# Kernel tuning notes

Measured on AMD Instinct MI355X. Metric: run time of the kernel, lower is better.

## Reference

```python
import jax, jax.numpy as jnp
import numpy as np

DIM = 48
HEADS = 8
DIM1 = DIM * HEADS  # 384
RED = 16


def setup_inputs() -> dict:
    key = jax.random.key(0)
    ks = jax.random.split(key, 10)
    s = 0.02
    return {
        "x": jax.random.normal(ks[0], (4, DIM, 128, 128), dtype=jnp.float32),
        "qkv_w": jax.random.normal(ks[1], (DIM1 * 4, DIM), dtype=jnp.float32) * s,
        "dw_w": jax.random.normal(ks[2], (DIM1 * 4, HEADS, 3, 3), dtype=jnp.float32) * s,  # groups=DIM*4 -> 8 in-ch per group
        "po1_w": jax.random.normal(ks[3], (DIM, DIM1), dtype=jnp.float32) * s,
        "fc1_w": jax.random.normal(ks[4], (DIM1 // RED, DIM1), dtype=jnp.float32) * s,
        "fc1_b": jnp.zeros((DIM1 // RED,), dtype=jnp.float32),
        "fc2_w": jax.random.normal(ks[5], (DIM1, DIM1 // RED), dtype=jnp.float32) * s,
        "fc2_b": jnp.zeros((DIM1,), dtype=jnp.float32),
        "temperature": jnp.ones((HEADS, 1, 1), dtype=jnp.float32),
    }


def reference(x, qkv_w, dw_w, po1_w, fc1_w, fc1_b, fc2_w, fc2_b, temperature):
    b, c, h, w = x.shape  # c == dim
    heads = temperature.shape[0]
    # 1x1 pointwise conv: dim -> dim1*4
    qkv = jnp.einsum('bchw,oc->bohw', x, qkv_w)
    # grouped 3x3 conv, groups = dim*4 (8 channels per group)
    qkv = jax.lax.conv_general_dilated(
        qkv, dw_w, window_strides=(1, 1), padding='SAME',
        feature_group_count=c * 4,
        dimension_numbers=('NCHW', 'OIHW', 'NCHW'))
    q, k, v, l = jnp.split(qkv, 4, axis=1)  # each (b, dim1, h, w)
    hw = h * w
    q = q.reshape(b, heads, c, hw)
    k = k.reshape(b, heads, c, hw)
    v = v.reshape(b, heads, c, hw)
    # ChannelAttention on l: note it returns fc2_out * sigmoid(fc2_out)
    avg = jnp.mean(l, axis=(2, 3))  # (b, dim1)
    y = jax.nn.relu(avg @ fc1_w.T + fc1_b)
    y = y @ fc2_w.T + fc2_b  # (b, dim1)
    L = (y * jax.nn.sigmoid(y))[:, :, None, None]  # (b, dim1, 1, 1)
    # L2-normalize over spatial (last) axis, torch eps=1e-12
    q = q / jnp.clip(jnp.linalg.norm(q, axis=-1, keepdims=True), 1e-12)
    k = k / jnp.clip(jnp.linalg.norm(k, axis=-1, keepdims=True), 1e-12)
    # channel-wise attention: (b, heads, c, c)
    attn = jnp.einsum('bhcn,bhdn->bhcd', q, k) * temperature
    attn = jax.nn.softmax(attn, axis=-1)
    out = jnp.einsum('bhcd,bhdn->bhcn', attn, v).reshape(b, heads * c, h, w)
    out = L + out
    out = jnp.einsum('bchw,oc->bohw', out, po1_w) + x
    return out
```

## Files before the change

### kernel.cpp

```cpp
#include <hip/hip_runtime.h>
#include <cstdint>

#define BB 4
#define CC 48
#define HW 16384
#define D1 384
#define HEADS 8

typedef unsigned short ushort_t;
typedef __attribute__((ext_vector_type(8))) short short8;
typedef __attribute__((ext_vector_type(4))) float f32x4;

__device__ __forceinline__ float bf2f(ushort_t u){
  union{uint32_t i; float f;} v; v.i = ((uint32_t)u)<<16; return v.f;
}
__device__ __forceinline__ ushort_t f2bf(float f){
  union{float f; uint32_t i;} v; v.f=f;
  uint32_t x = v.i;
  uint32_t r = (x + 0x7fff + ((x>>16)&1)) >> 16;
  return (ushort_t)r;
}

__global__ __launch_bounds__(256) void k_wf(const float* __restrict__ dw,
                                            const float* __restrict__ qw,
                                            ushort_t* __restrict__ wfp,
                                            float* __restrict__ qn2){
  int oc = blockIdx.x, tid = threadIdx.x;
  if(oc < 19){ int i = oc*256 + tid; if(i < 4800) qn2[i] = 0.f; }
  int slice = oc>>7, oc128 = oc&127;
  int mhalf = oc128>>6, oc64 = oc128&63;
  int mt = oc64>>4, mrow = oc64&15;
  for(int kk=tid; kk<448; kk+=256){
    int t = kk/48, c = kk - t*48;
    float s = 0.f;
    if(t < 9){
      #pragma unroll
      for(int j=0;j<8;j++)
        s += dw[(size_t)oc*72 + j*9 + t] * qw[(size_t)((oc>>3)*8 + j)*48 + c];
    }
    int chunk = kk>>5, rem = kk&31, quad = rem>>3, j = rem&7;
    size_t addr = ((((size_t)(slice*2+mhalf)*14 + chunk)*4 + mt)*64 + quad*16 + mrow)*8 + j;
    wfp[addr] = f2bf(s);
  }
}

__global__ __launch_bounds__(256) void k_xpose(const float* __restrict__ x,
                                               ushort_t* __restrict__ xb16,
                                               float* __restrict__ xst){
  int gy = blockIdx.x;
  int b  = blockIdx.y;
  ushort_t* orow = xb16 + ((size_t)b*130 + gy)*130*48;
  int tid = threadIdx.x;
  if(gy==0 || gy==129){
    short8 z = {0,0,0,0,0,0,0,0};
    for(int u=tid; u<780; u+=256) *(short8*)(orow + u*8) = z;
    return;
  }
  __shared__ float xl[48*128];
  const float* xr = x + (size_t)b*CC*HW + (size_t)(gy-1)*128;
  for(int i=tid;i<6144;i+=256){
    int c=i>>7, p=i&127;
    xl[c*128+p] = xr[(size_t)c*HW + p];
  }
  __syncthreads();
  for(int u=tid; u<780; u+=256){
    int gx = u/6, s = u-gx*6;
    ushort_t tmp[8];
    if(gx==0||gx==129){
      #pragma unroll
      for(int j=0;j<8;j++) tmp[j]=0;
    } else {
      #pragma unroll
      for(int j=0;j<8;j++) tmp[j] = f2bf(xl[(s*8+j)*128 + (gx-1)]);
    }
    *(short8*)(orow + (size_t)u*8) = *(short8*)tmp;
  }
  if(tid < 48){
    const float* row = &xl[tid*128];
    float a0=0,a1=0,a2=0,a3=0;
    #pragma unroll 8
    for(int p=0;p<128;p+=4){ a0+=row[p]; a1+=row[p+1]; a2+=row[p+2]; a3+=row[p+3]; }
    float s = (a0+a1)+(a2+a3);
    float* o = xst + ((size_t)b*48 + tid)*9;
    atomicAdd(&o[0], s);
    atomicAdd(&o[3], row[0]);
    atomicAdd(&o[4], row[127]);
    if(gy==1)  { o[1]=s; o[5]=row[0]; o[6]=row[127]; }
    if(gy==128){ o[2]=s; o[7]=row[0]; o[8]=row[127]; }
  }
}

#define HROWC 64
__global__ __launch_bounds__(256,4) void k_conv(const ushort_t* __restrict__ xb16,
                                                const ushort_t* __restrict__ wfp,
                                                ushort_t* __restrict__ qkvd){
  __shared__ __align__(16) ushort_t xs[180*HROWC];
  int tid  = threadIdx.x;
  int wave = tid>>6, lane = tid&63;
  int quad = lane>>4, mrow = lane&15;
  int mhalf = wave>>1, nhalf = wave&1;
  int tile = blockIdx.x;
  int ty0 = (tile>>3)*8, tx0 = (tile&7)*16;
  int ocb = blockIdx.y*128 + mhalf*64;
  int b   = blockIdx.z;

  {
    const ushort_t* xh = xb16 + ((size_t)b*16900 + (size_t)ty0*130 + tx0)*48;
    short8 vbuf[8];
    #pragma unroll
    for(int i=0;i<8;i++){
      int u = tid + i*256;
      int uu = (u < 1944) ? u : 1943;
      int r = uu/6, g = uu - r*6;
      int hy = r/18, hx = r - hy*18;
      vbuf[i] = *(const short8*)(xh + ((size_t)hy*130 + hx)*48 + g*8);
    }
    #pragma unroll
    for(int i=0;i<8;i++){
      int u = tid + i*256;
      if(u < 1944){
        int r = u/6, g = u - r*6;
        *(short8*)(xs + r*HROWC + ((g ^ (r&7))<<3)) = vbuf[i];
      }
    }
  }
  __syncthreads();

  int rb[4];
  #pragma unroll
  for(int nt=0;nt<4;nt++) rb[nt] = (nhalf*4+nt+1)*18 + mrow + 1;

  const ushort_t* AbF = wfp + ((size_t)(blockIdx.y*2 + mhalf)*14*4)*512 + lane*8;
  f32x4 Cacc[4][4];
  #pragma unroll
  for(int mt=0;mt<4;mt++)
    #pragma unroll
    for(int nt=0;nt<4;nt++) Cacc[mt][nt] = (f32x4){0.f,0.f,0.f,0.f};

  #pragma unroll
  for(int chunk=0; chunk<14; chunk++){
    short8 Ac[4];
    #pragma unroll
    for(int mt=0;mt<4;mt++)
      Ac[mt] = *(const short8*)(AbF + (size_t)(chunk*4 + mt)*512);
    int kq = chunk*32 + quad*8;
    int t  = kq/48;
    int c  = kq - t*48;
    int tc = (t<9) ? t : 8;
    int dyq = tc/3;
    int drow = dyq*18 + (tc - dyq*3) - 19;
    int g = c>>3;
    short8 Bf[4];
    #pragma unroll
    for(int nt=0;nt<4;nt++){
      int r = rb[nt] + drow;
      Bf[nt] = *(const short8*)(xs + r*HROWC + ((g ^ (r&7))<<3));
    }
    #pragma unroll
    for(int mt=0;mt<4;mt++)
      #pragma unroll
      for(int nt=0;nt<4;nt++)
        Cacc[mt][nt] = __builtin_amdgcn_mfma_f32_16x16x32_bf16(Bf[nt], Ac[mt], Cacc[mt][nt], 0,0,0);
  }

  #pragma unroll
  for(int mt=0;mt<4;mt++){
    int oc = ocb + mt*16 + mrow;
    ushort_t* orow = qkvd + ((size_t)b*1152 + oc)*HW;
    #pragma unroll
    for(int nt=0;nt<4;nt++){
      int py = nhalf*4 + nt;
      int gpos = (ty0+py)*128 + tx0 + quad*4;
      ushort_t pk[4];
      #pragma unroll
      for(int r=0;r<4;r++) pk[r] = f2bf(Cacc[mt][nt][r]);
      *(uint2*)(orow + gpos) = *(uint2*)pk;
    }
  }
}

__global__ __launch_bounds__(256,3) void k_S(const ushort_t* __restrict__ qkvd,
                                             float* __restrict__ Spart,
                                             float* __restrict__ qn2){
  __shared__ __align__(16) ushort_t qk[96*264];
  int tid = threadIdx.x;
  int blk = blockIdx.x, h = blockIdx.y, b = blockIdx.z;
  int wave = tid>>6, lane = tid&63;
  int quad = lane>>4, mrow = lane&15;
  const ushort_t* qb = qkvd + ((size_t)b*1152 + h*48)*HW;
  const ushort_t* kb = qb + (size_t)384*HW;

  f32x4 accS[3][3], accq[3], acck[3];
  #pragma unroll
  for(int mt=0;mt<3;mt++){
    accq[mt] = (f32x4){0.f,0.f,0.f,0.f};
    acck[mt] = (f32x4){0.f,0.f,0.f,0.f};
    #pragma unroll
    for(int nt=0;nt<3;nt++) accS[mt][nt] = (f32x4){0.f,0.f,0.f,0.f};
  }

  for(int half=0; half<2; half++){
    int p0 = blk*512 + half*256;
    __syncthreads();
    for(int u=tid; u<3072; u+=256){
      int ch = u>>5, px = u&31;
      const ushort_t* src = ((ch<48) ? qb + (size_t)ch*HW
                                     : kb + (size_t)(ch-48)*HW) + p0 + px*8;
      *(short8*)(qk + ch*264 + px*8) = *(const short8*)src;
    }
    __syncthreads();
    #pragma unroll
    for(int ks=0; ks<2; ks++){
      int koff = wave*64 + ks*32 + quad*8;
      short8 Aq[3], Bk[3];
      #pragma unroll
      for(int mt=0;mt<3;mt++) Aq[mt] = *(const short8*)(qk + (mt*16+mrow)*264 + koff);
      #pragma unroll
      for(int nt=0;nt<3;nt++) Bk[nt] = *(const short8*)(qk + (48+nt*16+mrow)*264 + koff);
      #pragma unroll
      for(int mt=0;mt<3;mt++){
        accq[mt] = __builtin_amdgcn_mfma_f32_16x16x32_bf16(Aq[mt], Aq[mt], accq[mt], 0,0,0);
        acck[mt] = __builtin_amdgcn_mfma_f32_16x16x32_bf16(Bk[mt], Bk[mt], acck[mt], 0,0,0);
        #pragma unroll
        for(int nt=0;nt<3;nt++)
          accS[mt][nt] = __builtin_amdgcn_mfma_f32_16x16x32_bf16(Aq[mt], Bk[nt], accS[mt][nt], 0,0,0);
      }
    }
  }
  __syncthreads();
  float* scr = (float*)qk;
  #pragma unroll
  for(int mt=0;mt<3;mt++)
    #pragma unroll
    for(int nt=0;nt<3;nt++)
      #pragma unroll
      for(int r=0;r<4;r++)
        scr[wave*2304 + (mt*16+quad*4+r)*48 + nt*16 + mrow] = accS[mt][nt][r];
  __syncthreads();
  float* outp = Spart + ((size_t)((b*HEADS+h)*32 + blk))*2304;
  for(int idx=tid; idx<2304; idx+=256)
    outp[idx] = scr[idx] + scr[2304+idx] + scr[4608+idx] + scr[6912+idx];
  int rr = mrow - (quad<<2);
  #pragma unroll
  for(int r=0;r<4;r++){
    if(rr == r){
      #pragma unroll
      for(int mt=0;mt<3;mt++){
        atomicAdd(qn2 + (size_t)b*D1 + h*48 + mt*16 + mrow, accq[mt][r]);
        atomicAdd(qn2 + 1536 + (size_t)b*D1 + h*48 + mt*16 + mrow, acck[mt][r]);
      }
    }
  }
}

__global__ __launch_bounds__(384) void k_mlp(const float* __restrict__ xst,
                                             const float* __restrict__ qw,
                                             const float* __restrict__ dw,
                                             const float* __restrict__ fc1w,
                                             const float* __restrict__ fc1b,
                                             const float* __restrict__ fc2w,
                                             const float* __restrict__ fc2b,
                                             const float* __restrict__ po1,
                                             float* __restrict__ constv){
  int b = blockIdx.x, tid = threadIdx.x;
  __shared__ float xsl[432];
  __shared__ float lst[3456];
  __shared__ float avg[384];
  __shared__ float y1[24];
  __shared__ float Lb[384];
  for(int i=tid;i<432;i+=384) xsl[i] = xst[(size_t)b*432 + i];
  __syncthreads();
  {
    float st[9];
    #pragma unroll
    for(int s=0;s<9;s++) st[s]=0.f;
    const float* w = qw + (size_t)(1152+tid)*48;
    for(int c=0;c<48;c++){
      float wv = w[c];
      #pragma unroll
      for(int s=0;s<9;s++) st[s] += wv*xsl[c*9+s];
    }
    #pragma unroll
    for(int s=0;s<9;s++) lst[tid*9+s] = st[s];
  }
  __syncthreads();
  {
    int base = tid & ~7;
    const float* ls = &lst[base*9];
    float s = 0.f;
    #pragma unroll
    for(int i=0;i<8;i++){
      float T=ls[i*9+0],R0=ls[i*9+1],R1=ls[i*9+2],C0=ls[i*9+3],C1=ls[i*9+4];
      float c00=ls[i*9+5],c0W=ls[i*9+6],cH0=ls[i*9+7],cHW=ls[i*9+8];
      const float* wp = dw + (size_t)(1152+tid)*72 + i*9;
      #pragma unroll
      for(int dy=0;dy<3;dy++){
        float rm = (dy==0)?R1:((dy==2)?R0:0.f);
        #pragma unroll
        for(int dx=0;dx<3;dx++){
          float cm = (dx==0)?C1:((dx==2)?C0:0.f);
          float corner = 0.f;
          if(dy==0&&dx==0)corner=cHW;
          if(dy==0&&dx==2)corner=cH0;
          if(dy==2&&dx==0)corner=c0W;
          if(dy==2&&dx==2)corner=c00;
          s += wp[dy*3+dx]*(T-rm-cm+corner);
        }
      }
    }
    avg[tid] = s*(1.f/16384.f);
  }
  __syncthreads();
  if(tid<24){
    float s = fc1b[tid];
    const float* w = fc1w + (size_t)tid*384;
    for(int c=0;c<384;c++) s += w[c]*avg[c];
    y1[tid] = fmaxf(s,0.f);
  }
  __syncthreads();
  {
    float s = fc2b[tid];
    const float* w = fc2w + (size_t)tid*24;
    #pragma unroll
    for(int j=0;j<24;j++) s += w[j]*y1[j];
    Lb[tid] = s/(1.f+__expf(-s));
  }
  __syncthreads();
  if(tid<48){
    const float* w = po1 + (size_t)tid*384;
    float s = 0.f;
    for(int c=0;c<384;c++) s += w[c]*Lb[c];
    constv[b*48+tid] = s;
  }
}

__global__ __launch_bounds__(256) void k_attn(const float* __restrict__ Spart,
                                              const float* __restrict__ qn2,
                                              const float* __restrict__ temp,
                                              const float* __restrict__ po1,
                                              ushort_t* __restrict__ m2o){
  int h = blockIdx.x, b = blockIdx.y, tid = threadIdx.x;
  __shared__ float att[2304];
  __shared__ float nq[48], nk[48];
  const float* kn2 = qn2 + 1536;
  if(tid<48)      nq[tid]    = fmaxf(sqrtf(qn2[(size_t)b*D1 + h*48 + tid]),    1e-12f);
  else if(tid<96) nk[tid-48] = fmaxf(sqrtf(kn2[(size_t)b*D1 + h*48 + tid-48]), 1e-12f);
  __syncthreads();
  float tmp = temp[h];
  const float* Sp = Spart + ((size_t)(b*HEADS+h)*32)*2304;
  for(int idx=tid; idx<2304; idx+=256){
    float s = 0.f;
    for(int blk=0;blk<32;blk++) s += Sp[(size_t)blk*2304 + idx];
    int c = idx/48, d = idx - c*48;
    att[idx] = s*tmp/(nq[c]*nk[d]);
  }
  __syncthreads();
  if(tid<48){
    float* row = &att[tid*48];
    float m = -1e30f;
    for(int d=0;d<48;d++) m = fmaxf(m,row[d]);
    float s = 0.f;
    for(int d=0;d<48;d++){ float e=__expf(row[d]-m); row[d]=e; s+=e; }
    float inv = 1.f/s;
    for(int d=0;d<48;d++) row[d]*=inv;
  }
  __syncthreads();
  for(int idx=tid; idx<2304; idx+=256){
    int d = idx/48, o = idx - d*48;
    float s = 0.f;
    for(int c=0;c<48;c++) s += po1[(size_t)o*D1 + h*48 + c]*att[c*48+d];
    int hd = h*48 + d;
    int ck = hd>>5, rem = hd&31, quad = rem>>3, j = rem&7;
    int mt = o>>4, mrow = o&15;
    m2o[((((size_t)b*12 + ck)*3 + mt)*64 + quad*16 + mrow)*8 + j] = f2bf(s);
  }
}

#define FROW2 40
__global__ __launch_bounds__(256,4) void k_final(const ushort_t* __restrict__ qkvd,
                                                 const ushort_t* __restrict__ m2o,
                                                 const float* __restrict__ constv,
                                                 const float* __restrict__ x,
                                                 float* __restrict__ out){
  __shared__ __align__(16) ushort_t vT[2][64*FROW2];
  int tid = threadIdx.x;
  int wave = tid>>6, lane = tid&63;
  int quad = lane>>4, mrow = lane&15;
  int pos0 = blockIdx.x*64;
  int b = blockIdx.y;
  const ushort_t* vb = qkvd + ((size_t)b*1152 + 768)*HW + pos0;
  const ushort_t* AbF = m2o + (size_t)b*18432 + lane*8;
  f32x4 acc[3];
  #pragma unroll
  for(int mt=0;mt<3;mt++) acc[mt] = (f32x4){0.f,0.f,0.f,0.f};

  auto stage = [&](int ck, int buf){
    int ch = tid>>3, pg = tid&7, p0 = pg*8;
    int chg = ch>>3, cl = ch&7;
    short8 v = *(const short8*)(vb + (size_t)(ck*32+ch)*HW + p0);
    ushort_t tmp[8]; *(short8*)tmp = v;
    #pragma unroll
    for(int i=0;i<8;i++){
      int p = p0+i;
      int sl = (chg ^ (p&3) ^ ((p>>3)&3)) & 3;
      vT[buf][p*FROW2 + (sl<<3) + cl] = tmp[i];
    }
  };
  stage(0,0);
  __syncthreads();
  for(int ck=0; ck<12; ck++){
    if(ck<11) stage(ck+1, (ck+1)&1);
    short8 Af[3], Bf;
    #pragma unroll
    for(int mt=0;mt<3;mt++)
      Af[mt] = *(const short8*)(AbF + (size_t)(ck*3 + mt)*512);
    {
      int p = wave*16 + mrow;
      int sl = (quad ^ (p&3) ^ ((p>>3)&3)) & 3;
      Bf = *(const short8*)(&vT[ck&1][p*FROW2 + (sl<<3)]);
    }
    #pragma unroll
    for(int mt=0;mt<3;mt++)
      acc[mt] = __builtin_amdgcn_mfma_f32_16x16x32_bf16(Af[mt], Bf, acc[mt], 0,0,0);
    __syncthreads();
  }
  const float* xb = x + (size_t)b*CC*HW + pos0;
  float* ob = out + (size_t)b*CC*HW + pos0;
  #pragma unroll
  for(int mt=0;mt<3;mt++){
    int p = wave*16 + mrow;
    #pragma unroll
    for(int r=0;r<4;r++){
      int o = mt*16 + quad*4 + r;
      ob[(size_t)o*HW + p] = xb[(size_t)o*HW + p] + constv[b*48+o] + acc[mt][r];
    }
  }
}

extern "C" void kernel_launch(void* const* d_in, const int* in_sizes, int n_in,
                              void* d_out, int out_size, void* d_ws, size_t ws_size,
                              hipStream_t stream){
  const float* x    = (const float*)d_in[0];
  const float* qw   = (const float*)d_in[1];
  const float* dw   = (const float*)d_in[2];
  const float* po1  = (const float*)d_in[3];
  const float* fc1w = (const float*)d_in[4];
  const float* fc1b = (const float*)d_in[5];
  const float* fc2w = (const float*)d_in[6];
  const float* fc2b = (const float*)d_in[7];
  const float* temp = (const float*)d_in[8];
  float* out = (float*)d_out;
  char* ws = (char*)d_ws;

  ushort_t* qkvd   = (ushort_t*)(ws);
  float*    Spart  = (float*)(ws + 150994944);
  ushort_t* xb16   = (ushort_t*)(ws + 150994944);
  float*    qn2    = (float*)(ws + 160432128);
  float*    xst    = (float*)(ws + 160444416);
  float*    constv = (float*)(ws + 160451328);
  ushort_t* m2o    = (ushort_t*)(ws + 160452096);
  ushort_t* wfp    = (ushort_t*)(ws + 160599552);

  k_wf    <<<dim3(1152),         256, 0, stream>>>(dw, qw, wfp, qn2);
  k_xpose <<<dim3(130,BB),       256, 0, stream>>>(x, xb16, xst);
  k_conv  <<<dim3(128,9,BB),     256, 0, stream>>>(xb16, wfp, qkvd);
  k_S     <<<dim3(32,HEADS,BB),  256, 0, stream>>>(qkvd, Spart, qn2);
  k_mlp   <<<dim3(BB),           384, 0, stream>>>(xst, qw, dw, fc1w, fc1b, fc2w, fc2b, po1, constv);
  k_attn  <<<dim3(HEADS,BB),     256, 0, stream>>>(Spart, qn2, temp, po1, m2o);
  k_final <<<dim3(256,BB),       256, 0, stream>>>(qkvd, m2o, constv, x, out);
}
```

Baseline: 303.4 us.

## Switch conv GEMM to 32x32x16 MFMA with register-prefetched weight fragments

Restructures the fused pointwise+3x3 conv GEMM in k_conv from 16x16x32 MFMA tiles, where each wave covered 64 oc by 64 pixels, to 32x32x16 tiles, where each wave covers 32 pixels by 128 output channels. The weight packing kernel is changed to match the new fragment layout. Weight fragments are now double-buffered in registers so the next chunk's global loads overlap the current MFMAs. Each wave now issues one LDS read per chunk instead of four, at the cost of more accumulator registers, which is why occupancy is lowered to 3 blocks per CU.

```diff
diff --git a/kernel.cpp b/kernel.cpp
--- a/kernel.cpp
+++ b/kernel.cpp
@@ -10,6 +10,7 @@
 typedef unsigned short ushort_t;
 typedef __attribute__((ext_vector_type(8))) short short8;
 typedef __attribute__((ext_vector_type(4))) float f32x4;
+typedef __attribute__((ext_vector_type(16))) float f32x16;
 
 __device__ __forceinline__ float bf2f(ushort_t u){
   union{uint32_t i; float f;} v; v.i = ((uint32_t)u)<<16; return v.f;
@@ -27,9 +28,8 @@
                                             float* __restrict__ qn2){
   int oc = blockIdx.x, tid = threadIdx.x;
   if(oc < 19){ int i = oc*256 + tid; if(i < 4800) qn2[i] = 0.f; }
-  int slice = oc>>7, oc128 = oc&127;
-  int mhalf = oc128>>6, oc64 = oc128&63;
-  int mt = oc64>>4, mrow = oc64&15;
+  int slice = oc>>7, ocl = oc&127;
+  int nt = ocl>>5, l31 = ocl&31;
   for(int kk=tid; kk<448; kk+=256){
     int t = kk/48, c = kk - t*48;
     float s = 0.f;
@@ -38,8 +38,8 @@
       for(int j=0;j<8;j++)
         s += dw[(size_t)oc*72 + j*9 + t] * qw[(size_t)((oc>>3)*8 + j)*48 + c];
     }
-    int chunk = kk>>5, rem = kk&31, quad = rem>>3, j = rem&7;
-    size_t addr = ((((size_t)(slice*2+mhalf)*14 + chunk)*4 + mt)*64 + quad*16 + mrow)*8 + j;
+    int chunk = kk>>4, kr = kk&15, lhalf = kr>>3, j = kr&7;
+    size_t addr = (((size_t)(slice*28 + chunk)*4 + nt)*512) + (size_t)(lhalf*32 + l31)*8 + j;
     wfp[addr] = f2bf(s);
   }
 }
@@ -91,17 +91,16 @@
 }
 
 #define HROWC 64
-__global__ __launch_bounds__(256,4) void k_conv(const ushort_t* __restrict__ xb16,
+__global__ __launch_bounds__(256,3) void k_conv(const ushort_t* __restrict__ xb16,
                                                 const ushort_t* __restrict__ wfp,
                                                 ushort_t* __restrict__ qkvd){
   __shared__ __align__(16) ushort_t xs[180*HROWC];
   int tid  = threadIdx.x;
   int wave = tid>>6, lane = tid&63;
-  int quad = lane>>4, mrow = lane&15;
-  int mhalf = wave>>1, nhalf = wave&1;
+  int l31 = lane&31, lhalf = lane>>5;
   int tile = blockIdx.x;
   int ty0 = (tile>>3)*8, tx0 = (tile&7)*16;
-  int ocb = blockIdx.y*128 + mhalf*64;
+  int slice = blockIdx.y;
   int b   = blockIdx.z;
 
   {
@@ -126,54 +125,54 @@
   }
   __syncthreads();
 
-  int rb[4];
-  #pragma unroll
-  for(int nt=0;nt<4;nt++) rb[nt] = (nhalf*4+nt+1)*18 + mrow + 1;
-
-  const ushort_t* AbF = wfp + ((size_t)(blockIdx.y*2 + mhalf)*14*4)*512 + lane*8;
-  f32x4 Cacc[4][4];
-  #pragma unroll
-  for(int mt=0;mt<4;mt++)
-    #pragma unroll
-    for(int nt=0;nt<4;nt++) Cacc[mt][nt] = (f32x4){0.f,0.f,0.f,0.f};
-
-  #pragma unroll
-  for(int chunk=0; chunk<14; chunk++){
-    short8 Ac[4];
-    #pragma unroll
-    for(int mt=0;mt<4;mt++)
-      Ac[mt] = *(const short8*)(AbF + (size_t)(chunk*4 + mt)*512);
-    int kq = chunk*32 + quad*8;
-    int t  = kq/48;
-    int c  = kq - t*48;
+  int p  = wave*32 + l31;
+  int py = p>>4, px = p&15;
+  int rb = (py+1)*18 + px + 1;
+
+  const ushort_t* BbF = wfp + (size_t)slice*(28*4*512) + (size_t)lane*8;
+  f32x16 Cacc[4];
+  #pragma unroll
+  for(int nt=0;nt<4;nt++)
+    #pragma unroll
+    for(int e=0;e<16;e++) Cacc[nt][e] = 0.f;
+
+  short8 Bc[4], Bn[4];
+  #pragma unroll
+  for(int nt=0;nt<4;nt++) Bc[nt] = *(const short8*)(BbF + (size_t)nt*512);
+
+  #pragma unroll
+  for(int chunk=0; chunk<28; chunk++){
+    if(chunk < 27){
+      #pragma unroll
+      for(int nt=0;nt<4;nt++)
+        Bn[nt] = *(const short8*)(BbF + (size_t)((chunk+1)*4 + nt)*512);
+    }
+    int t  = chunk/3;
     int tc = (t<9) ? t : 8;
-    int dyq = tc/3;
-    int drow = dyq*18 + (tc - dyq*3) - 19;
-    int g = c>>3;
-    short8 Bf[4];
-    #pragma unroll
-    for(int nt=0;nt<4;nt++){
-      int r = rb[nt] + drow;
-      Bf[nt] = *(const short8*)(xs + r*HROWC + ((g ^ (r&7))<<3));
-    }
-    #pragma unroll
-    for(int mt=0;mt<4;mt++)
-      #pragma unroll
-      for(int nt=0;nt<4;nt++)
-        Cacc[mt][nt] = __builtin_amdgcn_mfma_f32_16x16x32_bf16(Bf[nt], Ac[mt], Cacc[mt][nt], 0,0,0);
-  }
-
-  #pragma unroll
-  for(int mt=0;mt<4;mt++){
-    int oc = ocb + mt*16 + mrow;
+    int dy = tc/3, dx = tc - dy*3;
+    int drow = (dy-1)*18 + (dx-1);
+    int g = (chunk - t*3)*2 + lhalf;
+    int r = rb + drow;
+    short8 Af = *(const short8*)(xs + r*HROWC + ((g ^ (r&7))<<3));
+    #pragma unroll
+    for(int nt=0;nt<4;nt++)
+      Cacc[nt] = __builtin_amdgcn_mfma_f32_32x32x16_bf16(Af, Bc[nt], Cacc[nt], 0,0,0);
+    #pragma unroll
+    for(int nt=0;nt<4;nt++) Bc[nt] = Bn[nt];
+  }
+
+  #pragma unroll
+  for(int nt=0;nt<4;nt++){
+    int oc = slice*128 + nt*32 + l31;
     ushort_t* orow = qkvd + ((size_t)b*1152 + oc)*HW;
     #pragma unroll
-    for(int nt=0;nt<4;nt++){
-      int py = nhalf*4 + nt;
-      int gpos = (ty0+py)*128 + tx0 + quad*4;
+    for(int grp=0; grp<4; grp++){
+      int row = lhalf*4 + grp*8;
+      int pp  = wave*32 + row;
+      int gpos = (ty0 + (pp>>4))*128 + tx0 + (pp&15);
       ushort_t pk[4];
       #pragma unroll
-      for(int r=0;r<4;r++) pk[r] = f2bf(Cacc[mt][nt][r]);
+      for(int rr=0;rr<4;rr++) pk[rr] = f2bf(Cacc[nt][grp*4+rr]);
       *(uint2*)(orow + gpos) = *(uint2*)pk;
     }
   }
```

Measured after the change: 314.7 us. 3.7% more time.
